# Kernel optimization log

Hardware: AMD Instinct MI355X
Metric: run time of the kernel (lower is better)

Reference implementation:

```python
import jax, jax.numpy as jnp
import numpy as np

STRIDES = (8, 16, 32)
FMP = ((160, 160), (80, 80), (40, 40))
NUM_CLASSES = 80
TOPK = 1000
CONF_THRESH = 0.05
NMS_THRESH = 0.6
IMG_MAX = 1280.0
CLASS_OFFSET = 8192.0  # > any box coordinate, separates classes for batched NMS


def setup_inputs() -> dict:
    key = jax.random.key(0)
    ks = jax.random.split(key, 32)
    C = 256
    inp = {}
    for l, (h, w) in enumerate(FMP):
        inp[f'feat{l}'] = jax.random.normal(ks[l], (1, C, h, w), dtype=jnp.float32)
        inp[f'Wobj{l}'] = jax.random.normal(ks[3 + 6 * l + 0], (1, C), dtype=jnp.float32) * 0.05
        inp[f'bobj{l}'] = jnp.zeros((1,), dtype=jnp.float32)
        inp[f'Wcls{l}'] = jax.random.normal(ks[3 + 6 * l + 2], (NUM_CLASSES, C), dtype=jnp.float32) * 0.05
        inp[f'bcls{l}'] = jnp.zeros((NUM_CLASSES,), dtype=jnp.float32)
        inp[f'Wreg{l}'] = jax.random.normal(ks[3 + 6 * l + 4], (4, C), dtype=jnp.float32) * 0.05
        inp[f'breg{l}'] = jnp.zeros((4,), dtype=jnp.float32)
    return inp


def _level(feat, Wo, bo, Wc, bc, Wr, br, stride):
    x = feat[0]  # [C,H,W]
    H, W = x.shape[1], x.shape[2]
    def conv1x1(Wm, bv):
        # 1x1 conv == channel GEMM; output [H*W, O]
        return (jnp.einsum('oc,chw->hwo', Wm, x) + bv).reshape(H * W, -1)
    obj = conv1x1(Wo, bo)              # [M,1]
    cls = conv1x1(Wc, bc)              # [M,C]
    reg = jnp.exp(conv1x1(Wr, br)) * stride  # [M,4] (l,t,r,b)
    prob = jax.nn.sigmoid(obj) * jax.nn.sigmoid(cls)
    scores = prob.max(axis=-1)
    labels = prob.argmax(axis=-1)
    ay, ax = jnp.meshgrid(jnp.arange(H), jnp.arange(W), indexing='ij')
    anchors = (jnp.stack([ax, ay], axis=-1).astype(jnp.float32).reshape(-1, 2) + 0.5) * stride
    k = min(TOPK, H * W)
    scores, idx = jax.lax.top_k(scores, k)
    labels = labels[idx]
    reg = reg[idx]
    anchors = anchors[idx]
    boxes = jnp.concatenate([anchors - reg[:, :2], anchors + reg[:, 2:]], axis=-1)
    return scores, labels, boxes


def _batched_nms(boxes, scores, labels):
    N = boxes.shape[0]
    valid = scores >= CONF_THRESH
    # class-offset trick: per-class NMS == single NMS on disjoint offset boxes
    ob = boxes + labels.astype(boxes.dtype)[:, None] * CLASS_OFFSET
    order = jnp.argsort(-scores)
    b = ob[order]
    v = valid[order]
    x1, y1, x2, y2 = b[:, 0], b[:, 1], b[:, 2], b[:, 3]
    areas = (x2 - x1) * (y2 - y1)
    xx1 = jnp.maximum(x1[:, None], x1[None, :])
    yy1 = jnp.maximum(y1[:, None], y1[None, :])
    xx2 = jnp.minimum(x2[:, None], x2[None, :])
    yy2 = jnp.minimum(y2[:, None], y2[None, :])
    w = jnp.maximum(1e-10, xx2 - xx1)
    h = jnp.maximum(1e-10, yy2 - yy1)
    inter = w * h
    iou = inter / (areas[:, None] + areas[None, :] - inter + 1e-14)
    idxs = jnp.arange(N)
    def body(i, keep):
        sup = keep[i] & (iou[i] > NMS_THRESH) & (idxs > i)
        return keep & ~sup
    keep_sorted = jax.lax.fori_loop(0, N, body, v)
    keep = jnp.zeros(N, dtype=bool).at[order].set(keep_sorted)
    return keep


def reference(feat0, feat1, feat2,
              Wobj0, bobj0, Wcls0, bcls0, Wreg0, breg0,
              Wobj1, bobj1, Wcls1, bcls1, Wreg1, breg1,
              Wobj2, bobj2, Wcls2, bcls2, Wreg2, breg2):
    feats = (feat0, feat1, feat2)
    params = ((Wobj0, bobj0, Wcls0, bcls0, Wreg0, breg0),
              (Wobj1, bobj1, Wcls1, bcls1, Wreg1, breg1),
              (Wobj2, bobj2, Wcls2, bcls2, Wreg2, breg2))
    ss, ll, bb = [], [], []
    for l in range(3):
        s, lab, box = _level(feats[l], *params[l], STRIDES[l])
        ss.append(s); ll.append(lab); bb.append(box)
    scores = jnp.concatenate(ss)
    labels = jnp.concatenate(ll)
    boxes = jnp.concatenate(bb)
    keep = _batched_nms(boxes, scores, labels)
    bboxes = jnp.clip(boxes / IMG_MAX, 0.0, 1.0)
    return bboxes, scores, labels.astype(jnp.int32), keep
```

## Files before the change

### kernel.cpp

```cpp
#include <hip/hip_runtime.h>
#include <math.h>

#define NTOT   33600
#define NSEL   3000
#define CAND_CAP 8192
#define NWORDS 47
#define NROWS_PAD 3008
#define FCAP 4
#define NGRP 525
#define WPER 21760
#define NSLC 10
#define NTRI 1128
#define ZTOT 199612

struct P21 {
  const float* feat[3];
  const float* Wobj[3];
  const float* bobj[3];
  const float* Wcls[3];
  const float* bcls[3];
  const float* Wreg[3];
  const float* breg[3];
};

__device__ __forceinline__ void level_of_block(int b, int t, int& l, int& p, int& g, int& HW) {
  if (b < 100)      { l = 0; p = b * 256 + t;         g = p;          HW = 25600; }
  else if (b < 125) { l = 1; p = (b - 100) * 256 + t; g = 25600 + p;  HW = 6400;  }
  else              { l = 2; p = (b - 125) * 256 + t; g = 32000 + p;  HW = 1600;  }
}

__device__ __forceinline__ void level_of_group(int grp, int lane, int& l, int& p, int& g,
                                               int& HW, int& Wd, double& stride) {
  if (grp < 400)      { l = 0; p = grp * 64 + lane;         g = p;         HW = 25600; Wd = 160; stride = 8.0;  }
  else if (grp < 500) { l = 1; p = (grp - 400) * 64 + lane; g = 25600 + p; HW = 6400;  Wd = 80;  stride = 16.0; }
  else                { l = 2; p = (grp - 500) * 64 + lane; g = 32000 + p; HW = 1600;  Wd = 40;  stride = 32.0; }
}

__device__ __forceinline__ double sigmoid_d(double x) { return 1.0 / (1.0 + exp(-x)); }

__device__ __forceinline__ unsigned long long shfl64(unsigned long long v, int src) {
  unsigned lo = (unsigned)__shfl((int)(unsigned)(v & 0xFFFFFFFFull), src, 64);
  unsigned hi = (unsigned)__shfl((int)(unsigned)(v >> 32), src, 64);
  return (((unsigned long long)hi) << 32) | (unsigned long long)lo;
}

__global__ __launch_bounds__(256) void k_setup(P21 P, unsigned* __restrict__ zbase,
                                               double* __restrict__ W64) {
  int id = blockIdx.x * 256 + threadIdx.x;
  if (id < ZTOT) zbase[id] = 0;
  if (id < 3 * WPER) {
    int l = id / WPER, r = id - l * WPER;
    const float* src;
    if (r < 256)        src = P.Wobj[l] + r;
    else if (r < 1280)  src = P.Wreg[l] + (r - 256);
    else                src = P.Wcls[l] + (r - 1280);
    W64[id] = (double)(*src);
  }
}

__global__ __launch_bounds__(256) void k_conv_chunk(P21 P, const double* __restrict__ W64,
    double* __restrict__ obj_t, double* __restrict__ reg_t,
    double* __restrict__ cmax, int* __restrict__ clab) {
  int l, p, g, HW;
  level_of_block(blockIdx.x, threadIdx.x, l, p, g, HW);
  if (p >= HW) return;
  const int ch = blockIdx.y;
  const float* __restrict__ fp = P.feat[l] + p;
  const double* __restrict__ Wl = W64 + l * WPER;

  if (ch == 0) {
    const double* __restrict__ Wo = Wl;
    const double* __restrict__ Wr = Wl + 256;
    double accO = (double)P.bobj[l][0];
    double accR[4];
#pragma unroll
    for (int j = 0; j < 4; j++) accR[j] = (double)P.breg[l][j];
    for (int c = 0; c < 256; c += 16) {
      double xc[16];
#pragma unroll
      for (int u = 0; u < 16; u++) xc[u] = (double)fp[(c + u) * HW];
#pragma unroll
      for (int u = 0; u < 16; u++) {
        accO = fma(Wo[c + u], xc[u], accO);
#pragma unroll
        for (int j = 0; j < 4; j++)
          accR[j] = fma(Wr[j * 256 + c + u], xc[u], accR[j]);
      }
    }
    obj_t[g] = accO;
#pragma unroll
    for (int j = 0; j < 4; j++) reg_t[4 * g + j] = accR[j];
  } else {
    const int base = (ch - 1) * 8;
    const double* __restrict__ Wc = Wl + 1280 + base * 256;
    const float* __restrict__ bcls = P.bcls[l];
    double a[8];
#pragma unroll
    for (int j = 0; j < 8; j++) a[j] = (double)bcls[base + j];
    for (int c = 0; c < 256; c += 16) {
      double xc[16];
#pragma unroll
      for (int u = 0; u < 16; u++) xc[u] = (double)fp[(c + u) * HW];
#pragma unroll
      for (int u = 0; u < 16; u++) {
#pragma unroll
        for (int j = 0; j < 8; j++)
          a[j] = fma(Wc[j * 256 + c + u], xc[u], a[j]);
      }
    }
    double maxv = a[0]; int lab = base;
#pragma unroll
    for (int j = 1; j < 8; j++) if (a[j] > maxv) { maxv = a[j]; lab = base + j; }
    cmax[(ch - 1) * NTOT + g] = maxv;
    clab[(ch - 1) * NTOT + g] = lab;
  }
}

__global__ __launch_bounds__(64) void k_combine(
    const double* __restrict__ obj_t, const double* __restrict__ reg_t,
    const double* __restrict__ cmax, const int* __restrict__ clab,
    double* __restrict__ score_d, int* __restrict__ label_d,
    double* __restrict__ box_d, unsigned* __restrict__ hist) {
  int l, p, g, HW, Wd; double stride;
  level_of_group(blockIdx.x, threadIdx.x, l, p, g, HW, Wd, stride);

  double maxv = cmax[g]; int lab = clab[g];
#pragma unroll
  for (int k = 1; k < NSLC; k++) {
    double v = cmax[k * NTOT + g];
    int lb = clab[k * NTOT + g];
    if (v > maxv) { maxv = v; lab = lb; }
  }
  double score = sigmoid_d(obj_t[g]) * sigmoid_d(maxv);
  int h = p / Wd, w = p - h * Wd;
  double ax = ((double)w + 0.5) * stride;
  double ay = ((double)h + 0.5) * stride;
  double e0 = exp(reg_t[4 * g + 0]) * stride;
  double e1 = exp(reg_t[4 * g + 1]) * stride;
  double e2 = exp(reg_t[4 * g + 2]) * stride;
  double e3 = exp(reg_t[4 * g + 3]) * stride;

  score_d[g] = score;
  label_d[g] = lab;
  box_d[4 * g + 0] = ax - e0;
  box_d[4 * g + 1] = ay - e1;
  box_d[4 * g + 2] = ax + e2;
  box_d[4 * g + 3] = ay + e3;

  unsigned key = __float_as_uint((float)score);
  atomicAdd(&hist[l * 65536 + (key >> 16)], 1u);
}

__global__ __launch_bounds__(256) void k_scan(const unsigned* __restrict__ hist,
                                              unsigned* __restrict__ cutB) {
  int l = blockIdx.x;
  const unsigned* h = hist + l * 65536;
  __shared__ unsigned cs[256];
  __shared__ unsigned hb[256];
  __shared__ int s_chunk;
  __shared__ unsigned s_acc;
  int t = threadIdx.x;
  {
    const uint4* hp = (const uint4*)(h + t * 256);
    unsigned s = 0;
    for (int b = 0; b < 64; b++) { uint4 v = hp[b]; s += v.x + v.y + v.z + v.w; }
    cs[t] = s;
  }
  __syncthreads();
  if (t == 0) {
    unsigned acc = 0; int chunk = 0;
    for (int tt = 255; tt >= 0; tt--) {
      if (acc + cs[tt] >= 1000u) { chunk = tt; break; }
      acc += cs[tt];
    }
    s_chunk = chunk; s_acc = acc;
  }
  __syncthreads();
  int chunk = s_chunk;
  hb[t] = h[chunk * 256 + t];
  __syncthreads();
  if (t == 0) {
    unsigned acc = s_acc;
    unsigned B = (unsigned)(chunk * 256);
    for (int b = 255; b >= 0; b--) {
      unsigned c = hb[b];
      if (acc + c >= 1000u) { B = (unsigned)(chunk * 256 + b); break; }
      acc += c;
    }
    cutB[l] = B;
  }
}

__global__ __launch_bounds__(64) void k_compact(const double* __restrict__ score_d,
    const unsigned* __restrict__ cutB, unsigned* __restrict__ cnt,
    double* __restrict__ cand_s, int* __restrict__ cand_g) {
  int l, p, g, HW, Wd; double stride;
  level_of_group(blockIdx.x, threadIdx.x, l, p, g, HW, Wd, stride);
  double sc = score_d[g];
  unsigned key = __float_as_uint((float)sc);
  if ((key >> 16) >= cutB[l]) {
    unsigned pos = atomicAdd(&cnt[l], 1u);
    if (pos < CAND_CAP) {
      cand_s[l * CAND_CAP + pos] = sc;
      cand_g[l * CAND_CAP + pos] = g;
    }
  }
}

__global__ __launch_bounds__(256) void k_rank(const double* __restrict__ cand_s,
    const int* __restrict__ cand_g, const unsigned* __restrict__ cnt,
    const int* __restrict__ label_d, const double* __restrict__ box_d,
    double* __restrict__ sel_s, int* __restrict__ sel_lab, double* __restrict__ sel_box) {
  const int l = blockIdx.y;
  const int M = (int)min(cnt[l], (unsigned)CAND_CAP);
  if (blockIdx.x * 4 >= M) return;
  const int q = blockIdx.x * 4 + (threadIdx.x >> 6);
  const int lane = threadIdx.x & 63;
  const bool active = (q < M);

  double s = 0.0; int g = 0;
  if (active) { s = cand_s[l * CAND_CAP + q]; g = cand_g[l * CAND_CAP + q]; }

  int r = 0;
  if (active) {
    for (int j = lane; j < M; j += 64) {
      double sj = cand_s[l * CAND_CAP + j];
      int gj = cand_g[l * CAND_CAP + j];
      r += (sj > s) || (sj == s && gj < g);
    }
  }
#pragma unroll
  for (int off = 32; off > 0; off >>= 1) r += __shfl_down(r, off, 64);

  if (active && lane == 0 && r < 1000) {
    int o = l * 1000 + r;
    sel_s[o] = s;
    sel_lab[o] = label_d[g];
    sel_box[4 * o + 0] = box_d[4 * g + 0];
    sel_box[4 * o + 1] = box_d[4 * g + 1];
    sel_box[4 * o + 2] = box_d[4 * g + 2];
    sel_box[4 * o + 3] = box_d[4 * g + 3];
  }
}

__global__ __launch_bounds__(256) void k_order(const double* __restrict__ sel_s,
    const int* __restrict__ sel_lab, const double* __restrict__ sel_box,
    int* __restrict__ sortIdx, double* __restrict__ sbox, int* __restrict__ svalid) {
  const int i = blockIdx.x;
  const int t = threadIdx.x;
  const double s = sel_s[i];
  int r = 0;
  for (int j = t; j < NSEL; j += 256) {
    double sj = sel_s[j];
    r += (sj > s) || (sj == s && j < i);
  }
#pragma unroll
  for (int off = 32; off > 0; off >>= 1) r += __shfl_down(r, off, 64);
  __shared__ int wsum[4];
  if ((t & 63) == 0) wsum[t >> 6] = r;
  __syncthreads();
  if (t == 0) {
    int rr = wsum[0] + wsum[1] + wsum[2] + wsum[3];
    sortIdx[rr] = i;
    double off = (double)sel_lab[i] * 8192.0;
    sbox[4 * rr + 0] = sel_box[4 * i + 0] + off;
    sbox[4 * rr + 1] = sel_box[4 * i + 1] + off;
    sbox[4 * rr + 2] = sel_box[4 * i + 2] + off;
    sbox[4 * rr + 3] = sel_box[4 * i + 3] + off;
    svalid[rr] = (s >= 0.05) ? 1 : 0;
  }
}

__global__ __launch_bounds__(256) void k_mask(const double* __restrict__ sbox,
    unsigned long long* __restrict__ denseG, unsigned long long* __restrict__ diagG,
    unsigned short* __restrict__ entG, int* __restrict__ cntGi) {
  int k = blockIdx.x, rc = 0;
  while (k >= NWORDS - rc) { k -= NWORDS - rc; rc++; }
  const int w = rc + k;
  const int t = threadIdx.x, lane = t & 63, wk = t >> 6;
  const int rbase = rc * 64;
  __shared__ double rbox[256];
  {
    int idx = rbase * 4 + t;
    rbox[t] = (idx < NSEL * 4) ? sbox[idx] : 0.0;
  }
  const int j = w * 64 + lane;
  const bool jok = (j < NSEL);
  double bx1 = 0, by1 = 0, bx2 = 0, by2 = 0, arj = 0;
  if (jok) {
    bx1 = sbox[4 * j + 0]; by1 = sbox[4 * j + 1];
    bx2 = sbox[4 * j + 2]; by2 = sbox[4 * j + 3];
    arj = (bx2 - bx1) * (by2 - by1);
  }
  __syncthreads();
#pragma unroll
  for (int rr = 0; rr < 16; rr++) {
    const int ro = wk * 16 + rr;
    const int i = rbase + ro;
    if (i >= NSEL) break;
    double x1 = rbox[ro * 4 + 0], y1 = rbox[ro * 4 + 1];
    double x2 = rbox[ro * 4 + 2], y2 = rbox[ro * 4 + 3];
    double ar = (x2 - x1) * (y2 - y1);
    bool c = false;
    if (jok && j > i) {
      double xx1 = fmax(x1, bx1), yy1 = fmax(y1, by1);
      double xx2 = fmin(x2, bx2), yy2 = fmin(y2, by2);
      double ww = fmax(1e-10, xx2 - xx1);
      double hh = fmax(1e-10, yy2 - yy1);
      double inter = ww * hh;
      double iou = inter / (ar + arj - inter + 1e-14);
      c = iou > 0.6;
    }
    unsigned long long word = __ballot(c);
    if (lane == 0) {
      denseG[(size_t)i * 48 + w] = word;
      if (w == rc) diagG[i] = word;
      else if (word) {
        unsigned long long tt = word;
        while (tt) {
          int b = __builtin_ctzll(tt); tt &= tt - 1;
          int slot = atomicAdd(&cntGi[i], 1);
          if (slot < FCAP) entG[i * FCAP + slot] = (unsigned short)(w * 64 + b);
        }
      }
    }
  }
}

__global__ __launch_bounds__(256) void k_final(
    const unsigned long long* __restrict__ denseG, const unsigned long long* __restrict__ diagG,
    const unsigned short* __restrict__ entG, const int* __restrict__ cntGi,
    const int* __restrict__ svalid, const int* __restrict__ sortIdx,
    const double* __restrict__ sel_s, const int* __restrict__ sel_lab,
    const double* __restrict__ sel_box, float* __restrict__ out) {
  __shared__ unsigned long long diagL[NROWS_PAD];
  __shared__ unsigned short entL[NROWS_PAD * FCAP];
  __shared__ unsigned short cntL[NROWS_PAD];
  __shared__ unsigned long long validL[48];
  __shared__ unsigned long long hasWL[48];
  __shared__ unsigned long long keepWL[48];
  __shared__ unsigned char keepO[NROWS_PAD];
  const int t = threadIdx.x;
  const int lane = t & 63;

  for (int k = t; k < NSEL; k += 256) diagL[k] = diagG[k];
  for (int k = NSEL + t; k < NROWS_PAD; k += 256) diagL[k] = 0ull;
  uint2* e2 = (uint2*)entL; const uint2* eg2 = (const uint2*)entG;
  for (int k = t; k < NSEL; k += 256) e2[k] = eg2[k];
  for (int k = NSEL + t; k < NROWS_PAD; k += 256) { uint2 z; z.x = 0; z.y = 0; e2[k] = z; }
  for (int k = t; k < NSEL; k += 256) cntL[k] = (unsigned short)cntGi[k];
  for (int k = NSEL + t; k < NROWS_PAD; k += 256) cntL[k] = 0;
  for (int i0 = t; i0 < NROWS_PAD; i0 += 256) {
    bool f = (i0 < NSEL) && (svalid[i0] != 0);
    unsigned long long b = __ballot(f);
    if ((t & 63) == 0) validL[i0 >> 6] = b;
  }
  __syncthreads();

  if (t < 64) {
    for (int w = 0; w < NWORDS; w++) {
      int i = w * 64 + lane;
      bool f = (diagL[i] != 0ull) || (cntL[i] != 0);
      unsigned long long b = __ballot(f);
      if (lane == 0) hasWL[w] = b;
    }
    unsigned long long rem = 0ull;
    unsigned long long keep = 0ull;
    for (int w = 0; w < NWORDS; w++) {
      unsigned long long vw = validL[w];
      unsigned long long remw = shfl64(rem, w);
      unsigned long long win = vw & ~remw;
      unsigned long long work = hasWL[w];
      while (work) {
        int d = __builtin_ctzll(work); work &= work - 1;
        if ((win >> d) & 1ull) {
          int i = w * 64 + d;
          win &= ~diagL[i];
          int c = cntL[i];
          if (c > FCAP) {
            unsigned long long rowj = (lane < NWORDS) ? denseG[(size_t)i * 48 + lane] : 0ull;
            rem |= rowj;
          } else {
            for (int k = 0; k < c; k++) {
              int j = entL[i * FCAP + k];
              if ((j >> 6) == lane) rem |= 1ull << (j & 63);
            }
          }
        }
      }
      if (lane == w) keep = win;
    }
    if (lane < NWORDS) keepWL[lane] = keep;
  }
  __syncthreads();

  for (int r = t; r < NSEL; r += 256)
    keepO[sortIdx[r]] = (unsigned char)((keepWL[r >> 6] >> (r & 63)) & 1ull);
  __syncthreads();
  for (int i = t; i < NSEL; i += 256) {
#pragma unroll
    for (int c = 0; c < 4; c++) {
      double v = sel_box[4 * i + c] / 1280.0;
      v = fmin(fmax(v, 0.0), 1.0);
      out[4 * i + c] = (float)v;
    }
    out[12000 + i] = (float)sel_s[i];
    out[15000 + i] = (float)sel_lab[i];
    out[18000 + i] = keepO[i] ? 1.0f : 0.0f;
  }
}

extern "C" void kernel_launch(void* const* d_in, const int* in_sizes, int n_in,
                              void* d_out, int out_size, void* d_ws, size_t ws_size,
                              hipStream_t stream) {
  P21 P;
  for (int l = 0; l < 3; l++) {
    P.feat[l] = (const float*)d_in[7 * l + 0];
    P.Wobj[l] = (const float*)d_in[7 * l + 1];
    P.bobj[l] = (const float*)d_in[7 * l + 2];
    P.Wcls[l] = (const float*)d_in[7 * l + 3];
    P.bcls[l] = (const float*)d_in[7 * l + 4];
    P.Wreg[l] = (const float*)d_in[7 * l + 5];
    P.breg[l] = (const float*)d_in[7 * l + 6];
  }

  char* ws = (char*)d_ws;
  size_t off = 0;
  auto alloc = [&](size_t bytes) -> char* {
    char* p = ws + off;
    off += (bytes + 15) & ~(size_t)15;
    return p;
  };
  double* score_d  = (double*)alloc((size_t)NTOT * 8);
  double* box_d    = (double*)alloc((size_t)NTOT * 4 * 8);
  int*    label_d  = (int*)   alloc((size_t)NTOT * 4);
  double* obj_t    = (double*)alloc((size_t)NTOT * 8);
  double* reg_t    = (double*)alloc((size_t)NTOT * 4 * 8);
  double* cmax     = (double*)alloc((size_t)NSLC * NTOT * 8);
  int*    clab     = (int*)   alloc((size_t)NSLC * NTOT * 4);
  double* W64      = (double*)alloc((size_t)3 * WPER * 8);
  double* sel_s    = (double*)alloc((size_t)NSEL * 8);
  double* sel_box  = (double*)alloc((size_t)NSEL * 4 * 8);
  int*    sel_lab  = (int*)   alloc((size_t)NSEL * 4);
  int*    sortIdx  = (int*)   alloc((size_t)NSEL * 4);
  double* sbox     = (double*)alloc((size_t)NSEL * 4 * 8);
  int*    svalid   = (int*)   alloc((size_t)NSEL * 4);
  double* cand_s   = (double*)alloc((size_t)3 * CAND_CAP * 8);
  int*    cand_g   = (int*)   alloc((size_t)3 * CAND_CAP * 4);
  unsigned long long* denseG = (unsigned long long*)alloc((size_t)NSEL * 48 * 8);
  unsigned long long* diagG  = (unsigned long long*)alloc((size_t)NSEL * 8);
  unsigned short*     entG   = (unsigned short*)alloc((size_t)NSEL * FCAP * 2);
  unsigned* hist   = (unsigned*)alloc((size_t)3 * 65536 * 4);
  unsigned* cnt    = (unsigned*)alloc(16);
  int*      cntGi  = (int*)   alloc((size_t)NSEL * 4);
  unsigned* cutB   = (unsigned*)alloc(16);

  k_setup   <<<(ZTOT + 255) / 256, 256, 0, stream>>>(P, hist, W64);
  dim3 cgrid(132, 11, 1);
  k_conv_chunk<<<cgrid, 256, 0, stream>>>(P, W64, obj_t, reg_t, cmax, clab);
  k_combine <<<NGRP, 64, 0, stream>>>(obj_t, reg_t, cmax, clab, score_d, label_d, box_d, hist);
  k_scan    <<<3, 256, 0, stream>>>(hist, cutB);
  k_compact <<<NGRP, 64, 0, stream>>>(score_d, cutB, cnt, cand_s, cand_g);
  dim3 rgrid(CAND_CAP / 4, 3, 1);
  k_rank    <<<rgrid, 256, 0, stream>>>(cand_s, cand_g, cnt, label_d, box_d,
                                        sel_s, sel_lab, sel_box);
  k_order   <<<NSEL, 256, 0, stream>>>(sel_s, sel_lab, sel_box, sortIdx, sbox, svalid);
  k_mask    <<<NTRI, 256, 0, stream>>>(sbox, denseG, diagG, entG, cntGi);
  k_final   <<<1, 256, 0, stream>>>(denseG, diagG, entG, cntGi, svalid, sortIdx,
                                    sel_s, sel_lab, sel_box, (float*)d_out);
}
```

Measured before the change: 266.1 us.

## Stage feature tile in LDS and compute all conv outputs per block

The conv kernel is restructured so each 512-thread block loads a 64-pixel by 256-channel feature tile into shared memory once. Eight wavefronts then each compute 11 of the 85 output rows (obj, reg and class) from that tile. Before, 11 separate y-slices each re-read the features from global memory. Class partial maxima are reduced over 8 slices instead of 10. The rows per thread (11 double accumulators) add register pressure, fp64 FMAs now read weights per channel with scalar loads, and there are only 525 blocks.

New measurement: 458.0 us. 1.72x slower.

```diff
diff --git a/kernel.cpp b/kernel.cpp
--- a/kernel.cpp
+++ b/kernel.cpp
@@ -9,7 +9,7 @@
 #define FCAP 4
 #define NGRP 525
 #define WPER 21760
-#define NSLC 10
+#define NSLC 8
 #define NTRI 1128
 #define ZTOT 199612
 
@@ -22,12 +22,6 @@
   const float* Wreg[3];
   const float* breg[3];
 };
-
-__device__ __forceinline__ void level_of_block(int b, int t, int& l, int& p, int& g, int& HW) {
-  if (b < 100)      { l = 0; p = b * 256 + t;         g = p;          HW = 25600; }
-  else if (b < 125) { l = 1; p = (b - 100) * 256 + t; g = 25600 + p;  HW = 6400;  }
-  else              { l = 2; p = (b - 125) * 256 + t; g = 32000 + p;  HW = 1600;  }
-}
 
 __device__ __forceinline__ void level_of_group(int grp, int lane, int& l, int& p, int& g,
                                                int& HW, int& Wd, double& stride) {
@@ -58,61 +52,60 @@
   }
 }
 
-__global__ __launch_bounds__(256) void k_conv_chunk(P21 P, const double* __restrict__ W64,
+__global__ __launch_bounds__(512) void k_conv(P21 P, const double* __restrict__ W64,
     double* __restrict__ obj_t, double* __restrict__ reg_t,
     double* __restrict__ cmax, int* __restrict__ clab) {
-  int l, p, g, HW;
-  level_of_block(blockIdx.x, threadIdx.x, l, p, g, HW);
-  if (p >= HW) return;
-  const int ch = blockIdx.y;
-  const float* __restrict__ fp = P.feat[l] + p;
+  __shared__ float sF[256 * 64];
+  const int t = threadIdx.x, lane = t & 63, grp = t >> 6;
+  int l, p, g, HW, Wd; double stride;
+  level_of_group(blockIdx.x, lane, l, p, g, HW, Wd, stride);
+  const float* __restrict__ fp = P.feat[l] + (p - lane);
+  for (int k = 0; k < 32; k++) {
+    int c = grp + 8 * k;
+    sF[c * 64 + lane] = fp[c * HW + lane];
+  }
+  __syncthreads();
+
   const double* __restrict__ Wl = W64 + l * WPER;
-
-  if (ch == 0) {
-    const double* __restrict__ Wo = Wl;
-    const double* __restrict__ Wr = Wl + 256;
-    double accO = (double)P.bobj[l][0];
-    double accR[4];
-#pragma unroll
-    for (int j = 0; j < 4; j++) accR[j] = (double)P.breg[l][j];
-    for (int c = 0; c < 256; c += 16) {
-      double xc[16];
-#pragma unroll
-      for (int u = 0; u < 16; u++) xc[u] = (double)fp[(c + u) * HW];
-#pragma unroll
-      for (int u = 0; u < 16; u++) {
-        accO = fma(Wo[c + u], xc[u], accO);
-#pragma unroll
-        for (int j = 0; j < 4; j++)
-          accR[j] = fma(Wr[j * 256 + c + u], xc[u], accR[j]);
-      }
-    }
-    obj_t[g] = accO;
-#pragma unroll
-    for (int j = 0; j < 4; j++) reg_t[4 * g + j] = accR[j];
+  const int r0 = grp * 11;
+  const double* wrow[11];
+#pragma unroll
+  for (int j = 0; j < 11; j++) {
+    int r = r0 + j; if (r > 84) r = 84;
+    wrow[j] = Wl + r * 256;
+  }
+  double acc[11];
+#pragma unroll
+  for (int j = 0; j < 11; j++) {
+    int r = r0 + j; if (r > 84) r = 84;
+    double b;
+    if (r == 0)      b = (double)P.bobj[l][0];
+    else if (r < 5)  b = (double)P.breg[l][r - 1];
+    else             b = (double)P.bcls[l][r - 5];
+    acc[j] = b;
+  }
+  for (int c = 0; c < 256; c++) {
+    double x = (double)sF[c * 64 + lane];
+#pragma unroll
+    for (int j = 0; j < 11; j++) acc[j] = fma(wrow[j][c], x, acc[j]);
+  }
+
+  if (grp == 0) {
+    obj_t[g] = acc[0];
+#pragma unroll
+    for (int j = 0; j < 4; j++) reg_t[4 * g + j] = acc[1 + j];
+    double m = acc[5]; int lb = 0;
+#pragma unroll
+    for (int j = 6; j < 11; j++) if (acc[j] > m) { m = acc[j]; lb = j - 5; }
+    cmax[g] = m; clab[g] = lb;
   } else {
-    const int base = (ch - 1) * 8;
-    const double* __restrict__ Wc = Wl + 1280 + base * 256;
-    const float* __restrict__ bcls = P.bcls[l];
-    double a[8];
-#pragma unroll
-    for (int j = 0; j < 8; j++) a[j] = (double)bcls[base + j];
-    for (int c = 0; c < 256; c += 16) {
-      double xc[16];
-#pragma unroll
-      for (int u = 0; u < 16; u++) xc[u] = (double)fp[(c + u) * HW];
-#pragma unroll
-      for (int u = 0; u < 16; u++) {
-#pragma unroll
-        for (int j = 0; j < 8; j++)
-          a[j] = fma(Wc[j * 256 + c + u], xc[u], a[j]);
-      }
-    }
-    double maxv = a[0]; int lab = base;
-#pragma unroll
-    for (int j = 1; j < 8; j++) if (a[j] > maxv) { maxv = a[j]; lab = base + j; }
-    cmax[(ch - 1) * NTOT + g] = maxv;
-    clab[(ch - 1) * NTOT + g] = lab;
+    const int cbase = r0 - 5;
+    const int nv = (grp == 7) ? 8 : 11;
+    double m = acc[0]; int lb = cbase;
+#pragma unroll
+    for (int j = 1; j < 11; j++)
+      if (j < nv && acc[j] > m) { m = acc[j]; lb = cbase + j; }
+    cmax[grp * NTOT + g] = m; clab[grp * NTOT + g] = lb;
   }
 }
 
@@ -456,8 +449,7 @@
   unsigned* cutB   = (unsigned*)alloc(16);
 
   k_setup   <<<(ZTOT + 255) / 256, 256, 0, stream>>>(P, hist, W64);
-  dim3 cgrid(132, 11, 1);
-  k_conv_chunk<<<cgrid, 256, 0, stream>>>(P, W64, obj_t, reg_t, cmax, clab);
+  k_conv    <<<NGRP, 512, 0, stream>>>(P, W64, obj_t, reg_t, cmax, clab);
   k_combine <<<NGRP, 64, 0, stream>>>(obj_t, reg_t, cmax, clab, score_d, label_d, box_d, hist);
   k_scan    <<<3, 256, 0, stream>>>(hist, cutB);
   k_compact <<<NGRP, 64, 0, stream>>>(score_d, cutB, cnt, cand_s, cand_g);
```
